# Optimization experiments

Hardware: AMD Instinct MI355X
Metric: run time of the kernel (lower is better)

## Reference

```python
import jax, jax.numpy as jnp
import numpy as np

TEMPERATURE = 1.0          # max(args.matching_temperature=1.0, 1e-6)
CONSISTENCY_WEIGHT = 0.5   # max(args.matching_consistency_weight=0.5, 0.0)
EPS = 1e-6

N, M, D, K = 16384, 16384, 128, 5


def setup_inputs() -> dict:
    key = jax.random.key(0)
    k1, k2, k3 = jax.random.split(key, 3)
    query = jax.random.normal(k1, (N, D), dtype=jnp.float32)
    memory_bank = jax.random.normal(k2, (M, D), dtype=jnp.float32)
    # per-memory-entry neighbor scale (positive), as in _build_patch_library_statistics
    neighbor_scale_bank = jax.random.uniform(k3, (M,), dtype=jnp.float32) + 0.1
    return {"query": query, "memory_bank": memory_bank,
            "neighbor_scale_bank": neighbor_scale_bank, "k": K}


def reference(query, memory_bank, neighbor_scale_bank, k):
    # Euclidean cdist: [N, M]
    q2 = jnp.sum(query * query, axis=-1, keepdims=True)            # [N,1]
    m2 = jnp.sum(memory_bank * memory_bank, axis=-1)               # [M]
    d2 = q2 + m2 - 2.0 * (query @ memory_bank.T)                   # [N,M]
    dist = jnp.sqrt(jnp.maximum(d2, 1e-12))

    # torch.topk(largest=False) -> k smallest distances, ascending
    neg_d, knn_indices = jax.lax.top_k(-dist, k)                   # [N,k]
    knn_distances = -neg_d

    # adaptive_knn reduction (_reduce_knn_distances)
    weights = jax.nn.softmax(-knn_distances / TEMPERATURE, axis=1)
    weighted_distance = jnp.sum(weights * knn_distances, axis=1)   # [N]

    neighbor_scale = jnp.mean(neighbor_scale_bank[knn_indices], axis=1)  # [N]
    normalized_distance = weighted_distance / jnp.maximum(neighbor_scale, EPS)

    mean_d = jnp.mean(knn_distances, axis=1)
    std_d = jnp.sqrt(jnp.maximum(
        jnp.mean((knn_distances - mean_d[:, None]) ** 2, axis=1), 0.0))  # unbiased=False
    consistency = std_d / jnp.maximum(mean_d, EPS)

    return normalized_distance * (1.0 + CONSISTENCY_WEIGHT * consistency)
```

## Files before the change

kernel.cpp:

```cpp
#include <hip/hip_runtime.h>
#include <hip/hip_bf16.h>
#include <math.h>

#define N_Q 16384
#define N_M 16384
#define DIM 128
#define KNN 5
#define SPLITS 8
#define COLS_PER_SPLIT (N_M / SPLITS)
#define ITERS (COLS_PER_SPLIT / 128)
#define BROWS 128
#define TSEL 8
#define TSEL2 16
#define LLIST 4
#define BIGF 3.0e38f

typedef __bf16 bf16x8 __attribute__((ext_vector_type(8)));
typedef float f32x4 __attribute__((ext_vector_type(4)));

__device__ __forceinline__ void gl2lds16(const void* g, void* l) {
    __builtin_amdgcn_global_load_lds(
        (const __attribute__((address_space(1))) void*)g,
        (__attribute__((address_space(3))) void*)l, 16, 0, 0);
}

__device__ __forceinline__ unsigned umed3(unsigned a, unsigned b, unsigned c) {
    unsigned d;
    asm("v_med3_u32 %0, %1, %2, %3" : "=v"(d) : "v"(a), "v"(b), "v"(c));
    return d;
}

template <int D>
__device__ __forceinline__ void insD(unsigned (&L)[D], unsigned k) {
#pragma unroll
    for (int i = D - 1; i >= 1; --i) L[i] = umed3(L[i - 1], L[i], k);
    L[0] = min(L[0], k);
}

__global__ void prep_kernel(const float* __restrict__ q,
                            const float* __restrict__ mem,
                            float* __restrict__ q2, float* __restrict__ m2,
                            float* __restrict__ m2b,
                            __hip_bfloat16* __restrict__ qb,
                            __hip_bfloat16* __restrict__ mb) {
    int gt = blockIdx.x * blockDim.x + threadIdx.x;
    int wid = gt >> 6;
    int lane = gt & 63;
    bool isq = wid < N_Q;
    int r = isq ? wid : wid - N_Q;
    const float* src = (isq ? q : mem) + (size_t)r * DIM;
    __hip_bfloat16* bdst = (isq ? qb : mb) + (size_t)r * DIM;
    float2 v = reinterpret_cast<const float2*>(src)[lane];
    __hip_bfloat162 bv;
    bv.x = __float2bfloat16(v.x);
    bv.y = __float2bfloat16(v.y);
    reinterpret_cast<__hip_bfloat162*>(bdst)[lane] = bv;
    float s = fmaf(v.x, v.x, v.y * v.y);
#pragma unroll
    for (int off = 32; off > 0; off >>= 1) s += __shfl_down(s, off, 64);
    if (lane == 0) {
        if (isq) {
            q2[r] = s;
        } else {
            m2[r] = s;
            m2b[r] = s + 256.0f;
        }
    }
}

__global__ __launch_bounds__(256, 3) void knn_tops_kernel(
    const __hip_bfloat16* __restrict__ qb, const __hip_bfloat16* __restrict__ mb,
    const float* __restrict__ m2b, unsigned* __restrict__ candK) {
    __shared__ __align__(16) unsigned char smem[33280];
    const int tid = threadIdx.x;
    const int w = tid >> 6;
    const int lane = tid & 63;
    const int i16 = lane & 15;
    const int g = lane >> 4;
    const int row0 = blockIdx.x * BROWS;
    const int col0 = blockIdx.y * COLS_PER_SPLIT;

    bf16x8 afrag[2][4];
#pragma unroll
    for (int ti = 0; ti < 2; ++ti) {
        const __hip_bfloat16* qrow =
            qb + (size_t)(row0 + w * 32 + ti * 16 + i16) * DIM;
#pragma unroll
        for (int ks = 0; ks < 4; ++ks)
            afrag[ti][ks] = *reinterpret_cast<const bf16x8*>(qrow + ks * 32 + g * 8);
    }

    unsigned lst[8][LLIST];
#pragma unroll
    for (int rr = 0; rr < 8; ++rr)
#pragma unroll
        for (int j = 0; j < LLIST; ++j) lst[rr][j] = 0xFFFFFFFFu;

    const int lds_base = i16 * 256 + ((g ^ (i16 & 7)) << 4);
    int soff[8];
#pragma unroll
    for (int it = 0; it < 8; ++it) {
        int fg = w * 512 + it * 64 + lane;
        int c = fg >> 4, sg = fg & 15;
        int gk = (sg & 8) | ((sg ^ c) & 7);
        soff[it] = c * DIM + gk * 8;
    }
    const __hip_bfloat16* mbt = mb + (size_t)col0 * DIM;

    for (int t = 0; t < ITERS; ++t) {
        __syncthreads();
#pragma unroll
        for (int it = 0; it < 8; ++it)
            gl2lds16(mbt + soff[it], smem + w * 8192 + it * 1024);
        if (tid < 32) {
            float4 v = *reinterpret_cast<const float4*>(m2b + col0 + t * 128 + tid * 4);
            *reinterpret_cast<float4*>(smem + 32768 + tid * 16) = v;
        }
        mbt += 128 * DIM;
        __syncthreads();

        const float* m2f = (const float*)(smem + 32768);
#pragma unroll
        for (int half = 0; half < 2; ++half) {
#pragma unroll
            for (int cc = 0; cc < 2; ++cc) {
                f32x4 acc[2][2];
#pragma unroll
                for (int ti = 0; ti < 2; ++ti)
#pragma unroll
                    for (int c2 = 0; c2 < 2; ++c2)
                        acc[ti][c2] = (f32x4){0.f, 0.f, 0.f, 0.f};
#pragma unroll
                for (int ks = 0; ks < 4; ++ks) {
                    const unsigned char* bp =
                        smem + (lds_base ^ (ks << 6)) + half * 16384;
#pragma unroll
                    for (int c2 = 0; c2 < 2; ++c2) {
                        int ct = cc * 2 + c2;
                        bf16x8 bfr =
                            *reinterpret_cast<const bf16x8*>(bp + ct * 4096);
                        acc[0][c2] = __builtin_amdgcn_mfma_f32_16x16x32_bf16(
                            afrag[0][ks], bfr, acc[0][c2], 0, 0, 0);
                        acc[1][c2] = __builtin_amdgcn_mfma_f32_16x16x32_bf16(
                            afrag[1][ks], bfr, acc[1][c2], 0, 0, 0);
                    }
                }
                float m2v[2];
                unsigned colv[2];
#pragma unroll
                for (int c2 = 0; c2 < 2; ++c2) {
                    int ct = cc * 2 + c2;
                    m2v[c2] = m2f[half * 64 + ct * 16 + i16];
                    colv[c2] =
                        (unsigned)(col0 + t * 128 + half * 64 + ct * 16 + i16);
                }
#pragma unroll
                for (int ti = 0; ti < 2; ++ti) {
#pragma unroll
                    for (int r = 0; r < 4; ++r) {
                        const int rr = ti * 4 + r;
#pragma unroll
                        for (int c2 = 0; c2 < 2; ++c2) {
                            float sb = fmaf(-2.f, acc[ti][c2][r], m2v[c2]);
                            unsigned k =
                                (__float_as_uint(sb) & 0xFFFFC000u) | colv[c2];
                            insD(lst[rr], k);
                        }
                    }
                }
            }
        }
    }

    __syncthreads();

#pragma unroll
    for (int rr = 0; rr < 8; ++rr) {
        unsigned pv[LLIST];
#pragma unroll
        for (int j = 0; j < LLIST; ++j)
            pv[j] = (unsigned)__shfl_xor((int)lst[rr][j], 8, 64);
#pragma unroll
        for (int j = 0; j < LLIST; ++j) insD(lst[rr], pv[j]);
    }
    unsigned* MG = (unsigned*)smem;
    if (i16 < 8) {
#pragma unroll
        for (int rr = 0; rr < 8; ++rr) {
            int row = w * 32 + (rr >> 2) * 16 + g * 4 + (rr & 3);
#pragma unroll
            for (int j = 0; j < LLIST; ++j)
                MG[row * 33 + i16 * LLIST + j] = lst[rr][j];
        }
    }
    __syncthreads();
    if (tid < BROWS) {
        unsigned bk[TSEL];
#pragma unroll
        for (int j = 0; j < TSEL; ++j) bk[j] = 0xFFFFFFFFu;
        for (int c = 0; c < 32; ++c) {
            unsigned k = MG[tid * 33 + c];
            insD(bk, k);
        }
        size_t base = (size_t)(row0 + tid) * (SPLITS * TSEL) + blockIdx.y * TSEL;
        *reinterpret_cast<uint4*>(candK + base) =
            make_uint4(bk[0], bk[1], bk[2], bk[3]);
        *reinterpret_cast<uint4*>(candK + base + 4) =
            make_uint4(bk[4], bk[5], bk[6], bk[7]);
    }
}

__global__ void merge_kernel(const unsigned* __restrict__ candK,
                             int* __restrict__ candI2) {
    int row = blockIdx.x * blockDim.x + threadIdx.x;
    const unsigned* ck = candK + (size_t)row * (SPLITS * TSEL);
    unsigned v[TSEL2];
#pragma unroll
    for (int j = 0; j < TSEL2; ++j) v[j] = 0xFFFFFFFFu;
    for (int s4 = 0; s4 < 16; ++s4) {
        uint4 kk = reinterpret_cast<const uint4*>(ck)[s4];
        insD(v, kk.x);
        insD(v, kk.y);
        insD(v, kk.z);
        insD(v, kk.w);
    }
#pragma unroll
    for (int j = 0; j < TSEL2; ++j)
        candI2[(size_t)row * TSEL2 + j] = (int)(v[j] & 0x3FFFu);
}

__global__ __launch_bounds__(256) void finalize_kernel(
    const float* __restrict__ q, const float* __restrict__ mem,
    const float* __restrict__ q2, const float* __restrict__ m2,
    const int* __restrict__ candI2, const float* __restrict__ scaleb,
    float* __restrict__ out) {
    int wv = threadIdx.x >> 6, lane = threadIdx.x & 63;
    int n = blockIdx.x * 4 + wv;
    int cand = lane >> 2, qd = lane & 3;
    int ci = candI2[(size_t)n * TSEL2 + cand];
    const float4* qr = reinterpret_cast<const float4*>(q + (size_t)n * DIM) + qd * 8;
    const float4* mr = reinterpret_cast<const float4*>(mem + (size_t)ci * DIM) + qd * 8;
    float dot = 0.f;
#pragma unroll
    for (int k = 0; k < 8; ++k) {
        float4 a = qr[k], b = mr[k];
        dot = fmaf(a.x, b.x, fmaf(a.y, b.y, fmaf(a.z, b.z, fmaf(a.w, b.w, dot))));
    }
    dot += __shfl_xor(dot, 1, 64);
    dot += __shfl_xor(dot, 2, 64);
    float v = (qd == 0) ? (q2[n] + m2[ci] - 2.f * dot) : BIGF;

    float dk[KNN]; int ik[KNN];
#pragma unroll
    for (int r = 0; r < KNN; ++r) {
        float mv = v; int ml = lane;
#pragma unroll
        for (int off = 32; off > 0; off >>= 1) {
            float ov = __shfl_xor(mv, off, 64);
            int   ol = __shfl_xor(ml, off, 64);
            if (ov < mv || (ov == mv && ol < ml)) { mv = ov; ml = ol; }
        }
        dk[r] = sqrtf(fmaxf(mv, 1e-12f));
        ik[r] = __shfl(ci, ml, 64);
        if (lane == ml) v = BIGF;
    }
    if (lane == 0) {
        float dmin = dk[0];
        float se = 0.f, wd = 0.f, sm = 0.f, ssc = 0.f;
#pragma unroll
        for (int j = 0; j < KNN; ++j) {
            float e = expf(-(dk[j] - dmin));
            se += e;
            wd = fmaf(e, dk[j], wd);
            sm += dk[j];
            ssc += scaleb[ik[j]];
        }
        wd /= se;
        float scale = ssc * 0.2f;
        float nd = wd / fmaxf(scale, 1e-6f);
        float mean = sm * 0.2f;
        float var = 0.f;
#pragma unroll
        for (int j = 0; j < KNN; ++j) {
            float dd = dk[j] - mean;
            var = fmaf(dd, dd, var);
        }
        var *= 0.2f;
        float cons = sqrtf(var) / fmaxf(mean, 1e-6f);
        out[n] = nd * (1.f + 0.5f * cons);
    }
}

extern "C" void kernel_launch(void* const* d_in, const int* in_sizes, int n_in,
                              void* d_out, int out_size, void* d_ws,
                              size_t ws_size, hipStream_t stream) {
    const float* query  = (const float*)d_in[0];
    const float* mem    = (const float*)d_in[1];
    const float* scaleb = (const float*)d_in[2];
    float* out = (float*)d_out;

    float* q2 = (float*)d_ws;
    float* m2 = q2 + N_Q;
    float* m2b = m2 + N_M;
    __hip_bfloat16* qb = (__hip_bfloat16*)(m2b + N_M);
    __hip_bfloat16* mb = qb + (size_t)N_Q * DIM;
    unsigned* candK = (unsigned*)(mb + (size_t)N_M * DIM);
    int* candI2 = (int*)(candK + (size_t)N_Q * SPLITS * TSEL);

    prep_kernel<<<(N_Q + N_M) / 4, 256, 0, stream>>>(query, mem, q2, m2, m2b,
                                                     qb, mb);
    dim3 gridB(N_Q / BROWS, SPLITS);
    knn_tops_kernel<<<gridB, 256, 0, stream>>>(qb, mb, m2b, candK);
    merge_kernel<<<N_Q / 256, 256, 0, stream>>>(candK, candI2);
    finalize_kernel<<<N_Q / 4, 256, 0, stream>>>(query, mem, q2, m2, candI2,
                                                 scaleb, out);
}
```

Baseline: 204.2 us.

## Double-buffer memory tiles in LDS and fold norm bias into MFMA accumulator

The main loop now stages the next 128-column memory-bank tile into a second LDS buffer while computing on the current one, so global-to-LDS loads overlap with MFMA and top-k work. It also scales the bf16 memory bank by -2 during prep and starts each accumulator at the column's m2 bias, which removes the per-element fma in the selection epilogue. The m2 values are now read straight from global memory instead of through LDS. LDS use roughly doubles to 64KB per block, which may stop three blocks from fitting per CU as the launch bounds request, lowering occupancy.

```diff
diff --git a/kernel.cpp b/kernel.cpp
--- a/kernel.cpp
+++ b/kernel.cpp
@@ -51,9 +51,10 @@
     const float* src = (isq ? q : mem) + (size_t)r * DIM;
     __hip_bfloat16* bdst = (isq ? qb : mb) + (size_t)r * DIM;
     float2 v = reinterpret_cast<const float2*>(src)[lane];
+    float sc = isq ? 1.0f : -2.0f;
     __hip_bfloat162 bv;
-    bv.x = __float2bfloat16(v.x);
-    bv.y = __float2bfloat16(v.y);
+    bv.x = __float2bfloat16(sc * v.x);
+    bv.y = __float2bfloat16(sc * v.y);
     reinterpret_cast<__hip_bfloat162*>(bdst)[lane] = bv;
     float s = fmaf(v.x, v.x, v.y * v.y);
 #pragma unroll
@@ -71,7 +72,8 @@
 __global__ __launch_bounds__(256, 3) void knn_tops_kernel(
     const __hip_bfloat16* __restrict__ qb, const __hip_bfloat16* __restrict__ mb,
     const float* __restrict__ m2b, unsigned* __restrict__ candK) {
-    __shared__ __align__(16) unsigned char smem[33280];
+    __shared__ __align__(16) unsigned char bufA[32768];
+    __shared__ __align__(16) unsigned char bufB[32768];
     const int tid = threadIdx.x;
     const int w = tid >> 6;
     const int lane = tid & 63;
@@ -105,21 +107,25 @@
         int gk = (sg & 8) | ((sg ^ c) & 7);
         soff[it] = c * DIM + gk * 8;
     }
-    const __hip_bfloat16* mbt = mb + (size_t)col0 * DIM;
-
-    for (int t = 0; t < ITERS; ++t) {
-        __syncthreads();
+
+    auto stage = [&](unsigned char* buf, int t) {
+        const __hip_bfloat16* src = mb + (size_t)(col0 + t * 128) * DIM;
 #pragma unroll
         for (int it = 0; it < 8; ++it)
-            gl2lds16(mbt + soff[it], smem + w * 8192 + it * 1024);
-        if (tid < 32) {
-            float4 v = *reinterpret_cast<const float4*>(m2b + col0 + t * 128 + tid * 4);
-            *reinterpret_cast<float4*>(smem + 32768 + tid * 16) = v;
-        }
-        mbt += 128 * DIM;
-        __syncthreads();
-
-        const float* m2f = (const float*)(smem + 32768);
+            gl2lds16(src + soff[it], buf + w * 8192 + it * 1024);
+    };
+
+    auto compute = [&](const unsigned char* buf, int t) {
+        float m2r[8];
+        unsigned colv[8];
+#pragma unroll
+        for (int h = 0; h < 2; ++h)
+#pragma unroll
+            for (int c = 0; c < 4; ++c) {
+                int cl = col0 + t * 128 + h * 64 + c * 16 + i16;
+                m2r[h * 4 + c] = m2b[cl];
+                colv[h * 4 + c] = (unsigned)cl;
+            }
 #pragma unroll
         for (int half = 0; half < 2; ++half) {
 #pragma unroll
@@ -128,12 +134,14 @@
 #pragma unroll
                 for (int ti = 0; ti < 2; ++ti)
 #pragma unroll
-                    for (int c2 = 0; c2 < 2; ++c2)
-                        acc[ti][c2] = (f32x4){0.f, 0.f, 0.f, 0.f};
+                    for (int c2 = 0; c2 < 2; ++c2) {
+                        float m = m2r[half * 4 + cc * 2 + c2];
+                        acc[ti][c2] = (f32x4){m, m, m, m};
+                    }
 #pragma unroll
                 for (int ks = 0; ks < 4; ++ks) {
                     const unsigned char* bp =
-                        smem + (lds_base ^ (ks << 6)) + half * 16384;
+                        buf + (lds_base ^ (ks << 6)) + half * 16384;
 #pragma unroll
                     for (int c2 = 0; c2 < 2; ++c2) {
                         int ct = cc * 2 + c2;
@@ -145,15 +153,6 @@
                             afrag[1][ks], bfr, acc[1][c2], 0, 0, 0);
                     }
                 }
-                float m2v[2];
-                unsigned colv[2];
-#pragma unroll
-                for (int c2 = 0; c2 < 2; ++c2) {
-                    int ct = cc * 2 + c2;
-                    m2v[c2] = m2f[half * 64 + ct * 16 + i16];
-                    colv[c2] =
-                        (unsigned)(col0 + t * 128 + half * 64 + ct * 16 + i16);
-                }
 #pragma unroll
                 for (int ti = 0; ti < 2; ++ti) {
 #pragma unroll
@@ -161,15 +160,25 @@
                         const int rr = ti * 4 + r;
 #pragma unroll
                         for (int c2 = 0; c2 < 2; ++c2) {
-                            float sb = fmaf(-2.f, acc[ti][c2][r], m2v[c2]);
-                            unsigned k =
-                                (__float_as_uint(sb) & 0xFFFFC000u) | colv[c2];
+                            unsigned k = (__float_as_uint(acc[ti][c2][r]) &
+                                          0xFFFFC000u) |
+                                         colv[half * 4 + cc * 2 + c2];
                             insD(lst[rr], k);
                         }
                     }
                 }
             }
         }
+    };
+
+    stage(bufA, 0);
+    for (int t = 0; t < ITERS; t += 2) {
+        __syncthreads();
+        stage(bufB, t + 1);
+        compute(bufA, t);
+        __syncthreads();
+        if (t + 2 < ITERS) stage(bufA, t + 2);
+        compute(bufB, t + 1);
     }
 
     __syncthreads();
@@ -183,7 +192,7 @@
 #pragma unroll
         for (int j = 0; j < LLIST; ++j) insD(lst[rr], pv[j]);
     }
-    unsigned* MG = (unsigned*)smem;
+    unsigned* MG = (unsigned*)bufA;
     if (i16 < 8) {
 #pragma unroll
         for (int rr = 0; rr < 8; ++rr) {
```

New measurement: 203.1 us. Within noise of the previous version (-0.5%).
